# Optimization experiments

Hardware: AMD Instinct MI355X
Metric: run time of the kernel (lower is better)

The kernel has to match this reference:

```python
import jax, jax.numpy as jnp
import numpy as np

B, S, E, H = 2, 2048, 1024, 16
D = E // H  # head_dim = 64
EPS = 1e-6


def _angle_decay():
    # angle: 1/10000**linspace(0,1,D//2), each value repeated twice (interleaved)
    a = 1.0 / (10000.0 ** jnp.linspace(0.0, 1.0, D // 2))
    angle = jnp.repeat(a, 2)  # [D]
    decay = jnp.log(1.0 - 2.0 ** (-5.0 - jnp.arange(H, dtype=jnp.float32)))  # [H]
    return angle, decay


def _rel_pos(slen):
    angle, decay = _angle_decay()
    idx = jnp.arange(slen, dtype=jnp.float32)
    sin = jnp.sin(idx[:, None] * angle[None, :])  # [S, D]
    cos = jnp.cos(idx[:, None] * angle[None, :])  # [S, D]
    diff = idx[:, None] - idx[None, :]            # [S, S]
    tril = diff >= 0
    masked = jnp.where(tril, diff, jnp.inf)
    mask = jnp.exp(masked * decay[:, None, None])  # [H, S, S]; exp(-inf)=0 on upper tri
    mask = jnp.nan_to_num(mask)
    mask = mask / jnp.sqrt(jnp.sum(mask, axis=-1, keepdims=True))
    return sin, cos, mask


def _rotate_every_two(x):
    x1 = x[..., ::2]
    x2 = x[..., 1::2]
    return jnp.stack((-x2, x1), axis=-1).reshape(x.shape)


def _theta_shift(x, sin, cos):
    # x: [B, H, S, D]; sin/cos: [S, D] broadcast over B,H
    return x * cos + _rotate_every_two(x) * sin


def setup_inputs() -> dict:
    key = jax.random.key(0)
    ks = jax.random.split(key, 5)
    scale = 1.0 / np.sqrt(E)
    return {
        "x": jax.random.normal(ks[0], (B, S, E), dtype=jnp.float32),
        "Wq": jax.random.normal(ks[1], (E, E), dtype=jnp.float32) * scale,
        "Wk": jax.random.normal(ks[2], (E, E), dtype=jnp.float32) * scale,
        "Wv": jax.random.normal(ks[3], (E, E), dtype=jnp.float32) * scale,
        "Wg": jax.random.normal(ks[4], (E, E), dtype=jnp.float32) * scale,
    }


def reference(x, Wq, Wk, Wv, Wg):
    bsz, tgt_len, _ = x.shape
    sin, cos, mask = _rel_pos(tgt_len)
    scaling = E ** (-0.5)

    q = x @ Wq
    k = (x @ Wk) * scaling
    v = x @ Wv
    g = x @ Wg

    q = q.reshape(bsz, tgt_len, H, D).transpose(0, 2, 1, 3)  # [B,H,S,D]
    k = k.reshape(bsz, tgt_len, H, D).transpose(0, 2, 1, 3)
    vr = v.reshape(bsz, tgt_len, H, D).transpose(0, 2, 1, 3)

    qr = _theta_shift(q, sin, cos)
    kr = _theta_shift(k, sin, cos)

    qk = jnp.einsum("bhqd,bhkd->bhqk", qr, kr) * mask[None]
    denom = jax.lax.stop_gradient(
        jnp.clip(jnp.sum(jnp.abs(qk), axis=-1, keepdims=True), 1.0, 5e4)
    )
    out = jnp.einsum("bhqk,bhkd->bhqd", qk / denom, vr)
    out = out.transpose(0, 2, 1, 3)  # [B,S,H,D]

    # RMSNorm over head_dim (no affine)
    out = out * jax.lax.rsqrt(jnp.mean(out * out, axis=-1, keepdims=True) + EPS)
    out = out.reshape(bsz, tgt_len, E)
    return jax.nn.silu(g) * out
```

## Files before the change

### kernel.cpp

```cpp
#include <hip/hip_runtime.h>

typedef unsigned short u16;
typedef unsigned int u32;
typedef __attribute__((ext_vector_type(8))) __bf16 bf16x8;
typedef __attribute__((ext_vector_type(4))) float f32x4;

#define B_SZ   2
#define S_LEN  2048
#define E_DIM  1024
#define NHEAD  16
#define HD     64
#define KDIM   1024

__device__ __forceinline__ float bf2f(u16 u){
  union { u32 i; float f; } c; c.i = ((u32)u) << 16; return c.f;
}
__device__ __forceinline__ u16 f2bf(float f){
  union { float f; u32 i; } c; c.f = f;
  return (u16)((c.i + 0x7FFFu + ((c.i >> 16) & 1u)) >> 16);
}
__device__ __forceinline__ u16 f2bf_fast(float f){
  union { float f; u32 i; } c; c.f = f;
  return (u16)((c.i + 0x8000u) >> 16);
}
__device__ __forceinline__ void gl2lds16(const void* g, void* l){
  __builtin_amdgcn_global_load_lds((const __attribute__((address_space(1))) void*)g,
                                   (__attribute__((address_space(3))) void*)l, 16, 0, 0);
}

__global__ __launch_bounds__(256) void prep_kernel(const float* __restrict__ x,
                                                   const float* __restrict__ Wq, const float* __restrict__ Wk,
                                                   const float* __restrict__ Wv, const float* __restrict__ Wg,
                                                   u16* __restrict__ xb, u16* __restrict__ WT){
  __shared__ u16 tile[64][66];
  int z = blockIdx.z;
  int t = threadIdx.x;
  if (z < 4){
    const float* Ws[4] = {Wq, Wk, Wv, Wg};
    const float* W = Ws[z];
    int n0 = blockIdx.x * 64, k0 = blockIdx.y * 64;
    int r = t >> 2, cg = (t & 3) * 16;
    const float* src = W + (size_t)(k0 + r) * E_DIM + n0 + cg;
    float f[16];
    #pragma unroll
    for (int c = 0; c < 4; c++) *(float4*)&f[c * 4] = *(const float4*)&src[c * 4];
    #pragma unroll
    for (int i = 0; i < 16; i++) tile[r][cg + i] = f2bf(f[i]);
    __syncthreads();
    u16 ov[16];
    #pragma unroll
    for (int i = 0; i < 16; i++) ov[i] = tile[cg + i][r];
    int n7 = r & 7, cb = cg >> 3;
    u16* dst = WT + (size_t)(z * E_DIM + n0 + r) * KDIM + k0;
    *(uint4*)&dst[(cb ^ n7) * 8]       = *(uint4*)&ov[0];
    *(uint4*)&dst[((cb + 1) ^ n7) * 8] = *(uint4*)&ov[8];
  } else {
    int blk = (z - 4) * 256 + blockIdx.y * 16 + blockIdx.x;
    size_t flat = ((size_t)blk * 256 + t) * 16;
    int m7 = (int)((flat >> 10) & 7);
    int cb = (int)((flat >> 3) & 7);
    size_t tl = flat & ~(size_t)63;
    float f[16];
    #pragma unroll
    for (int c = 0; c < 4; c++) *(float4*)&f[c * 4] = *(const float4*)&x[flat + c * 4];
    u16 o[16];
    #pragma unroll
    for (int i = 0; i < 16; i++) o[i] = f2bf(f[i]);
    *(uint4*)&xb[tl + ((cb ^ m7) * 8)]       = *(uint4*)&o[0];
    *(uint4*)&xb[tl + (((cb + 1) ^ m7) * 8)] = *(uint4*)&o[8];
  }
}

__global__ __launch_bounds__(512, 2) void gemm_kernel(const u16* __restrict__ A, const u16* __restrict__ Bt,
                                                      u16* __restrict__ qr, u16* __restrict__ kr,
                                                      u16* __restrict__ vt, u16* __restrict__ gc){
  __shared__ __align__(16) u16 As[2][2][128 * 64];
  __shared__ __align__(16) u16 Bs[2][2][128 * 64];
  int m0 = blockIdx.y * 256, n0 = blockIdx.x * 256;
  int t = threadIdx.x;
  int wave = t >> 6, lane = t & 63;
  int l15 = lane & 15, quad = lane >> 4, h8 = lane & 7;
  int wm = wave >> 2, wn = wave & 3;

  f32x4 acc[8][4];
  #pragma unroll
  for (int i = 0; i < 8; i++)
    #pragma unroll
    for (int j = 0; j < 4; j++) acc[i][j] = (f32x4){0.f, 0.f, 0.f, 0.f};

  auto stA = [&](int buf, int half, int kt){
    const u16* src = A + (size_t)(m0 + half * 128) * KDIM + kt * 64;
    #pragma unroll
    for (int c = 0; c < 2; c++){
      int L = c * 512 + t;
      gl2lds16(src + (size_t)(L >> 3) * KDIM + (L & 7) * 8, &As[buf][half][L * 8]);
    }
  };
  auto stB = [&](int buf, int half, int kt){
    const u16* src = Bt + (size_t)(n0 + half * 128) * KDIM + kt * 64;
    #pragma unroll
    for (int c = 0; c < 2; c++){
      int L = c * 512 + t;
      gl2lds16(src + (size_t)(L >> 3) * KDIM + (L & 7) * 8, &Bs[buf][half][L * 8]);
    }
  };
  auto ldA = [&](int buf, int i, int ks) -> bf16x8 {
    int r = i * 16 + l15;
    return *(const bf16x8*)&As[buf][wm][r * 64 + (((ks * 4 + quad) ^ h8) * 8)];
  };
  auto ldB = [&](int buf, int j, int ks) -> bf16x8 {
    int c = (wn & 1) * 64 + j * 16 + l15;
    return *(const bf16x8*)&Bs[buf][wn >> 1][c * 64 + (((ks * 4 + quad) ^ h8) * 8)];
  };

  stA(0, 0, 0); stB(0, 0, 0); stA(0, 1, 0); stB(0, 1, 0);
  asm volatile("s_waitcnt vmcnt(4)" ::: "memory");
  __builtin_amdgcn_s_barrier();

  bf16x8 a[4][2];
  bf16x8 bA[2][2];
  bf16x8 bB[2][2];

  for (int t2 = 0; t2 < 8; ++t2){
    int kt0 = 2 * t2;
    bool more = (t2 < 7);

    #pragma unroll
    for (int half = 0; half < 2; ++half){
      int buf = half;
      bool stg = (buf == 0) || more;
      {
        #pragma unroll
        for (int i = 0; i < 4; i++){ a[i][0] = ldA(buf, i, 0); a[i][1] = ldA(buf, i, 1); }
        #pragma unroll
        for (int j = 0; j < 2; j++){ bA[j][0] = ldB(buf, j, 0); bA[j][1] = ldB(buf, j, 1); }
        if (buf == 0){ stA(1, 0, kt0 + 1); stB(1, 0, kt0 + 1); }
        else if (more){ stA(0, 0, kt0 + 2); stB(0, 0, kt0 + 2); }
        __builtin_amdgcn_sched_barrier(0);
        __builtin_amdgcn_s_barrier();
        asm volatile("s_waitcnt lgkmcnt(0)" ::: "memory");
        __builtin_amdgcn_sched_barrier(0);
        __builtin_amdgcn_s_setprio(1);
        #pragma unroll
        for (int i = 0; i < 4; i++)
          #pragma unroll
          for (int j = 0; j < 2; j++){
            acc[i][j] = __builtin_amdgcn_mfma_f32_16x16x32_bf16(a[i][0], bA[j][0], acc[i][j], 0, 0, 0);
            acc[i][j] = __builtin_amdgcn_mfma_f32_16x16x32_bf16(a[i][1], bA[j][1], acc[i][j], 0, 0, 0);
          }
        __builtin_amdgcn_s_setprio(0);
        __builtin_amdgcn_sched_barrier(0);
        if (stg) { asm volatile("s_waitcnt vmcnt(4)" ::: "memory"); }
        else     { asm volatile("s_waitcnt vmcnt(0)" ::: "memory"); }
        __builtin_amdgcn_s_barrier();
      }
      {
        #pragma unroll
        for (int j = 0; j < 2; j++){ bB[j][0] = ldB(buf, j + 2, 0); bB[j][1] = ldB(buf, j + 2, 1); }
        if (buf == 0){ stA(1, 1, kt0 + 1); stB(1, 1, kt0 + 1); }
        else if (more){ stA(0, 1, kt0 + 2); stB(0, 1, kt0 + 2); }
        __builtin_amdgcn_sched_barrier(0);
        __builtin_amdgcn_s_barrier();
        asm volatile("s_waitcnt lgkmcnt(0)" ::: "memory");
        __builtin_amdgcn_sched_barrier(0);
        __builtin_amdgcn_s_setprio(1);
        #pragma unroll
        for (int i = 0; i < 4; i++)
          #pragma unroll
          for (int j = 0; j < 2; j++){
            acc[i][j + 2] = __builtin_amdgcn_mfma_f32_16x16x32_bf16(a[i][0], bB[j][0], acc[i][j + 2], 0, 0, 0);
            acc[i][j + 2] = __builtin_amdgcn_mfma_f32_16x16x32_bf16(a[i][1], bB[j][1], acc[i][j + 2], 0, 0, 0);
          }
        __builtin_amdgcn_s_setprio(0);
        __builtin_amdgcn_sched_barrier(0);
        __builtin_amdgcn_s_barrier();
      }
      {
        #pragma unroll
        for (int i = 0; i < 4; i++){ a[i][0] = ldA(buf, i + 4, 0); a[i][1] = ldA(buf, i + 4, 1); }
        __builtin_amdgcn_sched_barrier(0);
        __builtin_amdgcn_s_barrier();
        asm volatile("s_waitcnt lgkmcnt(0)" ::: "memory");
        __builtin_amdgcn_sched_barrier(0);
        __builtin_amdgcn_s_setprio(1);
        #pragma unroll
        for (int i = 0; i < 4; i++)
          #pragma unroll
          for (int j = 0; j < 2; j++){
            acc[i + 4][j + 2] = __builtin_amdgcn_mfma_f32_16x16x32_bf16(a[i][0], bB[j][0], acc[i + 4][j + 2], 0, 0, 0);
            acc[i + 4][j + 2] = __builtin_amdgcn_mfma_f32_16x16x32_bf16(a[i][1], bB[j][1], acc[i + 4][j + 2], 0, 0, 0);
          }
        #pragma unroll
        for (int i = 0; i < 4; i++)
          #pragma unroll
          for (int j = 0; j < 2; j++){
            acc[i + 4][j] = __builtin_amdgcn_mfma_f32_16x16x32_bf16(a[i][0], bA[j][0], acc[i + 4][j], 0, 0, 0);
            acc[i + 4][j] = __builtin_amdgcn_mfma_f32_16x16x32_bf16(a[i][1], bA[j][1], acc[i + 4][j], 0, 0, 0);
          }
        __builtin_amdgcn_s_setprio(0);
        __builtin_amdgcn_sched_barrier(0);
        if (stg) { asm volatile("s_waitcnt vmcnt(4)" ::: "memory"); }
        __builtin_amdgcn_s_barrier();
      }
    }
  }

  int zone = n0 >> 10;
  int n0l = n0 & 1023;
  int hh = (n0l >> 6) + wn;

  if (zone == 3){
    #pragma unroll
    for (int i = 0; i < 8; i++){
      int row = m0 + wm * 128 + i * 16 + quad * 4;
      #pragma unroll
      for (int j = 0; j < 4; j++){
        int e = n0l + wn * 64 + j * 16 + l15;
        #pragma unroll
        for (int r = 0; r < 4; r++)
          gc[(size_t)(row + r) * E_DIM + e] = f2bf(acc[i][j][r]);
      }
    }
  } else if (zone == 2){
    #pragma unroll
    for (int i = 0; i < 8; i++){
      int srow = m0 + wm * 128 + i * 16 + quad * 4;
      int b = srow >> 11, sb = srow & 2047;
      #pragma unroll
      for (int j = 0; j < 4; j++){
        int d = j * 16 + l15;
        size_t rowb = ((size_t)((b << 4) + hh) * HD + d) * S_LEN;
        u16 pk[4];
        #pragma unroll
        for (int r = 0; r < 4; r++) pk[r] = f2bf(acc[i][j][r]);
        u32 lo = (u32)pk[0] | ((u32)pk[1] << 16);
        u32 hi = (u32)pk[2] | ((u32)pk[3] << 16);
        size_t off = rowb + (size_t)(sb & ~63) + (size_t)(((((sb >> 3) & 7) ^ (d & 7)) << 3) + (sb & 7));
        *(uint2*)&vt[off] = make_uint2(lo, hi);
      }
    }
  } else {
    float scale = (zone == 1) ? 0.03125f : 1.0f;
    float sgn = (l15 & 1) ? 1.0f : -1.0f;
    #pragma unroll
    for (int j = 0; j < 4; j++){
      int d = j * 16 + l15;
      float af = exp2f(-(float)(d >> 1) * (13.287712379549449f / 31.0f));
      #pragma unroll
      for (int i = 0; i < 8; i++){
        int srow = m0 + wm * 128 + i * 16 + quad * 4;
        int b = srow >> 11, sbase = srow & 2047;
        size_t base = (size_t)((b << 4) + hh) * S_LEN;
        #pragma unroll
        for (int r = 0; r < 4; r++){
          int s = sbase + r;
          float vv = acc[i][j][r] * scale;
          float p = __shfl_xor(vv, 1);
          float sn, cs;
          __sincosf((float)s * af, &sn, &cs);
          float outv = vv * cs + sgn * p * sn;
          u16 ob = f2bf(outv);
          if (zone == 0){
            qr[(base + s) * HD + d] = ob;
          } else {
            kr[(base + s) * HD + (((((d >> 3) & 7) ^ (s & 7)) << 3) + (d & 7))] = ob;
          }
        }
      }
    }
  }
}

__global__ __launch_bounds__(256, 2) void retention_kernel(const u16* __restrict__ qr, const u16* __restrict__ kr,
                                                           const u16* __restrict__ vt,
                                                           u16* __restrict__ pO, u16* __restrict__ pBa){
  int bh = blockIdx.x;
  int qb = 15 - (int)blockIdx.y;
  int z  = blockIdx.z;
  int h = bh & 15;
  int q0 = qb * 128;
  __shared__ __align__(16) u16 Ks[2][64 * 64];
  __shared__ __align__(16) u16 Vs[2][64 * 64];
  __shared__ __align__(16) u16 Ps[128 * 72];
  int t = threadIdx.x, wave = t >> 6, lane = t & 63;
  int l15 = lane & 15, quad = lane >> 4, h8 = lane & 7;

  float decay = log1pf(-exp2f(-5.0f - (float)h));
  float negd = -decay;
  float estep = __expf(64.0f * negd);

  int qsE[2], rowb[2];
  #pragma unroll
  for (int e = 0; e < 2; e++){ rowb[e] = wave * 32 + e * 16; qsE[e] = q0 + rowb[e]; }

  bf16x8 qB[2][2];
  #pragma unroll
  for (int e = 0; e < 2; e++){
    size_t qrow = ((size_t)bh * S_LEN + qsE[e] + l15) * HD;
    qB[e][0] = *(const bf16x8*)&qr[qrow + quad * 8];
    qB[e][1] = *(const bf16x8*)&qr[qrow + 32 + quad * 8];
  }

  float win_f = 11.0f / negd;
  int win_i = (win_f > 2.1e9f) ? 0x7f000000 : (int)win_f;
  int nk = 2 * qb + 2;
  int z_lo = (z * nk) >> 2;
  int z_hi = (((z + 1) * nk) >> 2) - 1;
  int kb_lo = z_lo;
  {
    int jmin = q0 - win_i;
    if (jmin > z_lo * 64){ int wlo = jmin >> 6; kb_lo = wlo > z_lo ? wlo : z_lo; }
  }
  int k0s = kb_lo * 64;

  float em1d = expm1f(decay);
  float rfE[2]; int iE[2];
  #pragma unroll
  for (int e = 0; e < 2; e++){
    int i = qsE[e] + l15;
    iE[e] = i;
    float rowsum = expm1f((float)(i + 1) * decay) / em1d;
    rfE[e] = __expf((float)(i - k0s) * decay) * rsqrtf(rowsum);
  }
  float e1 = __expf(negd);
  float c16 = __expf(negd * 16.0f);
  float cbr[4];
  cbr[0] = __expf(negd * (float)(quad * 4));
  cbr[1] = cbr[0] * e1; cbr[2] = cbr[1] * e1; cbr[3] = cbr[2] * e1;

  f32x4 o[2][4];
  #pragma unroll
  for (int e = 0; e < 2; e++)
    #pragma unroll
    for (int dt = 0; dt < 4; dt++) o[e][dt] = (f32x4){0.f, 0.f, 0.f, 0.f};
  float babs[2] = {0.f, 0.f};

  const u16* krbh = kr + (size_t)bh * S_LEN * HD;
  const u16* vtbh = vt + (size_t)bh * HD * S_LEN;

  if (kb_lo <= z_hi){
    {
      int k0 = kb_lo * 64;
      #pragma unroll
      for (int c = 0; c < 2; c++){
        int L = c * 256 + t;
        gl2lds16(krbh + (size_t)k0 * HD + L * 8, &Ks[0][L * 8]);
      }
      #pragma unroll
      for (int c = 0; c < 2; c++){
        int L = c * 256 + t;
        gl2lds16(vtbh + (size_t)(L >> 3) * S_LEN + k0 + (L & 7) * 8, &Vs[0][L * 8]);
      }
    }
    __syncthreads();
    int cur = 0;
    for (int kb = kb_lo; kb <= z_hi; kb++){
      if (kb < z_hi){
        int k0n = (kb + 1) * 64;
        #pragma unroll
        for (int c = 0; c < 2; c++){
          int L = c * 256 + t;
          gl2lds16(krbh + (size_t)k0n * HD + L * 8, &Ks[cur ^ 1][L * 8]);
        }
        #pragma unroll
        for (int c = 0; c < 2; c++){
          int L = c * 256 + t;
          gl2lds16(vtbh + (size_t)(L >> 3) * S_LEN + k0n + (L & 7) * 8, &Vs[cur ^ 1][L * 8]);
        }
      }
      int k0 = kb * 64;
      const u16* KsC = &Ks[cur][0];
      const u16* VsC = &Vs[cur][0];

      bf16x8 kA0[4], kA1[4];
      #pragma unroll
      for (int ct = 0; ct < 4; ct++){
        int rw = (ct * 16 + l15) * 64;
        kA0[ct] = *(const bf16x8*)&KsC[rw + ((quad ^ h8) * 8)];
        kA1[ct] = *(const bf16x8*)&KsC[rw + (((quad + 4) ^ h8) * 8)];
      }
      #pragma unroll
      for (int e = 0; e < 2; e++){
        int qs = qsE[e];
        if (k0 <= qs + 15 && k0 + 63 >= qs - win_i){
          bool diag = (k0 + 64 > qs);
          float cf[4] = {cbr[0], cbr[1], cbr[2], cbr[3]};
          #pragma unroll
          for (int ct = 0; ct < 4; ct++){
            f32x4 zacc = (f32x4){0.f, 0.f, 0.f, 0.f};
            zacc = __builtin_amdgcn_mfma_f32_16x16x32_bf16(kA0[ct], qB[e][0], zacc, 0, 0, 0);
            zacc = __builtin_amdgcn_mfma_f32_16x16x32_bf16(kA1[ct], qB[e][1], zacc, 0, 0, 0);
            u16 pk[4];
            #pragma unroll
            for (int r = 0; r < 4; r++){
              float p = zacc[r] * (rfE[e] * cf[r]);
              if (diag && (k0 + ct * 16 + quad * 4 + r) > iE[e]) p = 0.f;
              babs[e] += fabsf(p);
              pk[r] = f2bf_fast(p);
              cf[r] *= c16;
            }
            u32 lo = (u32)pk[0] | ((u32)pk[1] << 16);
            u32 hi = (u32)pk[2] | ((u32)pk[3] << 16);
            *(uint2*)&Ps[(rowb[e] + l15) * 72 + ct * 16 + quad * 4] = make_uint2(lo, hi);
          }
        }
      }
      #pragma unroll
      for (int e = 0; e < 2; e++){
        int qs = qsE[e];
        if (k0 <= qs + 15 && k0 + 63 >= qs - win_i){
          bf16x8 pB0 = *(const bf16x8*)&Ps[(rowb[e] + l15) * 72 + quad * 8];
          bf16x8 pB1 = *(const bf16x8*)&Ps[(rowb[e] + l15) * 72 + 32 + quad * 8];
          #pragma unroll
          for (int dt = 0; dt < 4; dt++){
            int rw = (dt * 16 + l15) * 64;
            bf16x8 vA0 = *(const bf16x8*)&VsC[rw + ((quad ^ h8) * 8)];
            bf16x8 vA1 = *(const bf16x8*)&VsC[rw + (((quad + 4) ^ h8) * 8)];
            o[e][dt] = __builtin_amdgcn_mfma_f32_16x16x32_bf16(vA0, pB0, o[e][dt], 0, 0, 0);
            o[e][dt] = __builtin_amdgcn_mfma_f32_16x16x32_bf16(vA1, pB1, o[e][dt], 0, 0, 0);
          }
        }
      }
      #pragma unroll
      for (int e = 0; e < 2; e++) rfE[e] *= estep;
      __syncthreads();
      cur ^= 1;
    }
  }

  size_t slot = ((size_t)bh * 16 + qb) * 4 + z;
  u16* po = pO + slot * (4 * 128 * 16);
  #pragma unroll
  for (int e = 0; e < 2; e++){
    float bsum = babs[e];
    bsum += __shfl_xor(bsum, 16);
    bsum += __shfl_xor(bsum, 32);
    if (quad == 0) pBa[slot * 128 + rowb[e] + l15] = f2bf(bsum);
    #pragma unroll
    for (int dt = 0; dt < 4; dt++){
      u16 pk[4];
      #pragma unroll
      for (int r = 0; r < 4; r++) pk[r] = f2bf(o[e][dt][r]);
      *(uint2*)&po[(dt * 128 + rowb[e] + l15) * 16 + quad * 4] = *(uint2*)pk;
    }
  }
}

__global__ __launch_bounds__(128) void combine_kernel(const u16* __restrict__ pO, const u16* __restrict__ pBa,
                                                      const u16* __restrict__ gc, float* __restrict__ out){
  int bh = blockIdx.x, qb = blockIdx.y;
  int b = bh >> 4, h = bh & 15;
  int i = threadIdx.x;
  int s = qb * 128 + i;
  size_t s4 = ((size_t)bh * 16 + qb) * 4;
  float v[64];
  #pragma unroll
  for (int d = 0; d < 64; d++) v[d] = 0.f;
  float bsum = 0.f;
  #pragma unroll
  for (int z = 0; z < 4; z++){
    const u16* pz = pO + (s4 + z) * 8192;
    #pragma unroll
    for (int dt = 0; dt < 4; dt++){
      u16 a[16];
      *(uint4*)&a[0] = *(const uint4*)&pz[(dt * 128 + i) * 16];
      *(uint4*)&a[8] = *(const uint4*)&pz[(dt * 128 + i) * 16 + 8];
      #pragma unroll
      for (int c = 0; c < 16; c++) v[dt * 16 + c] += bf2f(a[c]);
    }
    bsum += bf2f(pBa[(s4 + z) * 128 + i]);
  }
  float dinv = 1.0f / fminf(fmaxf(bsum, 1.0f), 50000.0f);
  float ssq = 0.f;
  #pragma unroll
  for (int d = 0; d < 64; d++){ v[d] *= dinv; ssq += v[d] * v[d]; }
  float rms = rsqrtf(ssq * (1.0f / 64.0f) + 1e-6f);
  size_t gbase = ((size_t)b * S_LEN + s) * E_DIM + h * HD;
  u16 gu[64];
  #pragma unroll
  for (int c = 0; c < 8; c++) *(uint4*)&gu[c * 8] = *(const uint4*)&gc[gbase + c * 8];
  float ov[64];
  #pragma unroll
  for (int d = 0; d < 64; d++){
    float gv = bf2f(gu[d]);
    float sg = gv / (1.0f + __expf(-gv));
    ov[d] = v[d] * rms * sg;
  }
  float* obase = out + ((size_t)b * S_LEN + s) * E_DIM + h * HD;
  #pragma unroll
  for (int c = 0; c < 16; c++) *(float4*)&obase[c * 4] = *(float4*)&ov[c * 4];
}

extern "C" void kernel_launch(void* const* d_in, const int* in_sizes, int n_in,
                              void* d_out, int out_size, void* d_ws, size_t ws_size,
                              hipStream_t stream){
  const float* x  = (const float*)d_in[0];
  const float* Wq = (const float*)d_in[1];
  const float* Wk = (const float*)d_in[2];
  const float* Wv = (const float*)d_in[3];
  const float* Wg = (const float*)d_in[4];
  float* out = (float*)d_out;
  char* ws = (char*)d_ws;
  u16* xb  = (u16*)(ws);
  u16* WT  = (u16*)(ws + (8ull  << 20));
  u16* pO  = (u16*)(ws);
  u16* qrp = (u16*)(ws + (32ull << 20));
  u16* krp = (u16*)(ws + (40ull << 20));
  u16* vtp = (u16*)(ws + (48ull << 20));
  u16* gcp = (u16*)(ws + (56ull << 20));
  u16* pBa = (u16*)(ws + (64ull << 20));

  prep_kernel     <<<dim3(16, 16, 8),  256, 0, stream>>>(x, Wq, Wk, Wv, Wg, xb, WT);
  gemm_kernel     <<<dim3(16, 16),     512, 0, stream>>>(xb, WT, qrp, krp, vtp, gcp);
  retention_kernel<<<dim3(32, 16, 4),  256, 0, stream>>>(qrp, krp, vtp, pO, pBa);
  combine_kernel  <<<dim3(32, 16),     128, 0, stream>>>(pO, pBa, gcp, out);
}
```

Before: 191.2 us.

## Stage GEMM epilogue through LDS for coalesced 16-byte output stores

The GEMM epilogue now writes each wave's accumulator tile into a reused shared-memory region, then reads it back and issues coalesced 16-byte global stores for the q, k, v and g outputs, replacing scattered 2-byte and 8-byte stores. The RoPE sin/cos values are advanced by angle-addition recurrences instead of calling sincos for every element. To make the LDS reuse safe, the main loop's vmcnt waits are tightened to vmcnt(0), which may reduce load/compute overlap. The recurrence also adds some rounding drift compared with direct sincos.

```diff
diff --git a/kernel.cpp b/kernel.cpp
--- a/kernel.cpp
+++ b/kernel.cpp
@@ -74,8 +74,7 @@
 __global__ __launch_bounds__(512, 2) void gemm_kernel(const u16* __restrict__ A, const u16* __restrict__ Bt,
                                                       u16* __restrict__ qr, u16* __restrict__ kr,
                                                       u16* __restrict__ vt, u16* __restrict__ gc){
-  __shared__ __align__(16) u16 As[2][2][128 * 64];
-  __shared__ __align__(16) u16 Bs[2][2][128 * 64];
+  __shared__ __align__(16) u16 SH[65536];
   int m0 = blockIdx.y * 256, n0 = blockIdx.x * 256;
   int t = threadIdx.x;
   int wave = t >> 6, lane = t & 63;
@@ -88,12 +87,15 @@
     #pragma unroll
     for (int j = 0; j < 4; j++) acc[i][j] = (f32x4){0.f, 0.f, 0.f, 0.f};
 
+  auto Aoff = [&](int buf, int half) -> int { return (buf * 2 + half) * 8192; };
+  auto Boff = [&](int buf, int half) -> int { return 32768 + (buf * 2 + half) * 8192; };
+
   auto stA = [&](int buf, int half, int kt){
     const u16* src = A + (size_t)(m0 + half * 128) * KDIM + kt * 64;
     #pragma unroll
     for (int c = 0; c < 2; c++){
       int L = c * 512 + t;
-      gl2lds16(src + (size_t)(L >> 3) * KDIM + (L & 7) * 8, &As[buf][half][L * 8]);
+      gl2lds16(src + (size_t)(L >> 3) * KDIM + (L & 7) * 8, &SH[Aoff(buf, half) + L * 8]);
     }
   };
   auto stB = [&](int buf, int half, int kt){
@@ -101,20 +103,20 @@
     #pragma unroll
     for (int c = 0; c < 2; c++){
       int L = c * 512 + t;
-      gl2lds16(src + (size_t)(L >> 3) * KDIM + (L & 7) * 8, &Bs[buf][half][L * 8]);
+      gl2lds16(src + (size_t)(L >> 3) * KDIM + (L & 7) * 8, &SH[Boff(buf, half) + L * 8]);
     }
   };
   auto ldA = [&](int buf, int i, int ks) -> bf16x8 {
     int r = i * 16 + l15;
-    return *(const bf16x8*)&As[buf][wm][r * 64 + (((ks * 4 + quad) ^ h8) * 8)];
+    return *(const bf16x8*)&SH[Aoff(buf, wm) + r * 64 + (((ks * 4 + quad) ^ h8) * 8)];
   };
   auto ldB = [&](int buf, int j, int ks) -> bf16x8 {
     int c = (wn & 1) * 64 + j * 16 + l15;
-    return *(const bf16x8*)&Bs[buf][wn >> 1][c * 64 + (((ks * 4 + quad) ^ h8) * 8)];
+    return *(const bf16x8*)&SH[Boff(buf, wn >> 1) + c * 64 + (((ks * 4 + quad) ^ h8) * 8)];
   };
 
   stA(0, 0, 0); stB(0, 0, 0); stA(0, 1, 0); stB(0, 1, 0);
-  asm volatile("s_waitcnt vmcnt(4)" ::: "memory");
+  asm volatile("s_waitcnt vmcnt(0)" ::: "memory");
   __builtin_amdgcn_s_barrier();
 
   bf16x8 a[4][2];
@@ -150,8 +152,6 @@
           }
         __builtin_amdgcn_s_setprio(0);
         __builtin_amdgcn_sched_barrier(0);
-        if (stg) { asm volatile("s_waitcnt vmcnt(4)" ::: "memory"); }
-        else     { asm volatile("s_waitcnt vmcnt(0)" ::: "memory"); }
         __builtin_amdgcn_s_barrier();
       }
       {
@@ -199,45 +199,61 @@
           }
         __builtin_amdgcn_s_setprio(0);
         __builtin_amdgcn_sched_barrier(0);
-        if (stg) { asm volatile("s_waitcnt vmcnt(4)" ::: "memory"); }
+        if (stg) { asm volatile("s_waitcnt vmcnt(0)" ::: "memory"); }
         __builtin_amdgcn_s_barrier();
       }
     }
   }
 
+  __syncthreads();
+  u16* epi = SH + wave * 8192;
   int zone = n0 >> 10;
   int n0l = n0 & 1023;
   int hh = (n0l >> 6) + wn;
-
-  if (zone == 3){
-    #pragma unroll
-    for (int i = 0; i < 8; i++){
-      int row = m0 + wm * 128 + i * 16 + quad * 4;
-      #pragma unroll
-      for (int j = 0; j < 4; j++){
-        int e = n0l + wn * 64 + j * 16 + l15;
-        #pragma unroll
-        for (int r = 0; r < 4; r++)
-          gc[(size_t)(row + r) * E_DIM + e] = f2bf(acc[i][j][r]);
-      }
-    }
-  } else if (zone == 2){
-    #pragma unroll
-    for (int i = 0; i < 8; i++){
-      int srow = m0 + wm * 128 + i * 16 + quad * 4;
-      int b = srow >> 11, sb = srow & 2047;
-      #pragma unroll
-      for (int j = 0; j < 4; j++){
-        int d = j * 16 + l15;
-        size_t rowb = ((size_t)((b << 4) + hh) * HD + d) * S_LEN;
+  int b = m0 >> 11;
+  int s0f = (m0 & 2047) + wm * 128;
+
+  if (zone == 2){
+    #pragma unroll
+    for (int j = 0; j < 4; j++){
+      int d = j * 16 + l15;
+      #pragma unroll
+      for (int i = 0; i < 8; i++){
+        int cs0 = i * 2 + (quad >> 1);
         u16 pk[4];
         #pragma unroll
         for (int r = 0; r < 4; r++) pk[r] = f2bf(acc[i][j][r]);
-        u32 lo = (u32)pk[0] | ((u32)pk[1] << 16);
-        u32 hi = (u32)pk[2] | ((u32)pk[3] << 16);
-        size_t off = rowb + (size_t)(sb & ~63) + (size_t)(((((sb >> 3) & 7) ^ (d & 7)) << 3) + (sb & 7));
-        *(uint2*)&vt[off] = make_uint2(lo, hi);
-      }
+        *(uint2*)&epi[d * 128 + ((cs0 ^ (d & 7)) * 8) + (quad & 1) * 4] = *(uint2*)pk;
+      }
+    }
+    __syncthreads();
+    int dl = lane >> 4, cl = lane & 15;
+    size_t vbase = (size_t)((b << 4) + hh) * HD * S_LEN;
+    #pragma unroll
+    for (int it = 0; it < 16; it++){
+      int d = it * 4 + dl;
+      uint4 v = *(const uint4*)&epi[d * 128 + cl * 8];
+      *(uint4*)&vt[vbase + (size_t)d * S_LEN + s0f + cl * 8] = v;
+    }
+  } else if (zone == 3){
+    #pragma unroll
+    for (int j = 0; j < 4; j++){
+      int c0c = 2 * j + (l15 >> 3), o7 = l15 & 7;
+      #pragma unroll
+      for (int i = 0; i < 8; i++)
+        #pragma unroll
+        for (int r = 0; r < 4; r++){
+          int row = i * 16 + quad * 4 + r;
+          epi[row * 64 + ((c0c ^ (row & 7)) * 8) + o7] = f2bf(acc[i][j][r]);
+        }
+    }
+    __syncthreads();
+    int rl = lane >> 3, cl = lane & 7;
+    #pragma unroll
+    for (int it = 0; it < 16; it++){
+      int row = it * 8 + rl;
+      uint4 v = *(const uint4*)&epi[row * 64 + ((cl ^ (row & 7)) * 8)];
+      *(uint4*)&gc[(size_t)(m0 + wm * 128 + row) * E_DIM + n0l + wn * 64 + cl * 8] = v;
     }
   } else {
     float scale = (zone == 1) ? 0.03125f : 1.0f;
@@ -245,28 +261,37 @@
     #pragma unroll
     for (int j = 0; j < 4; j++){
       int d = j * 16 + l15;
+      int c0c = 2 * j + (l15 >> 3), o7 = l15 & 7;
       float af = exp2f(-(float)(d >> 1) * (13.287712379549449f / 31.0f));
-      #pragma unroll
-      for (int i = 0; i < 8; i++){
-        int srow = m0 + wm * 128 + i * 16 + quad * 4;
-        int b = srow >> 11, sbase = srow & 2047;
-        size_t base = (size_t)((b << 4) + hh) * S_LEN;
+      float cs, sn, ca1, sa1, cb, sb_;
+      __sincosf((float)(s0f + quad * 4) * af, &sn, &cs);
+      __sincosf(af, &sa1, &ca1);
+      __sincosf(13.0f * af, &sb_, &cb);
+      #pragma unroll
+      for (int i = 0; i < 8; i++)
         #pragma unroll
         for (int r = 0; r < 4; r++){
-          int s = sbase + r;
+          int row = i * 16 + quad * 4 + r;
           float vv = acc[i][j][r] * scale;
           float p = __shfl_xor(vv, 1);
-          float sn, cs;
-          __sincosf((float)s * af, &sn, &cs);
           float outv = vv * cs + sgn * p * sn;
-          u16 ob = f2bf(outv);
-          if (zone == 0){
-            qr[(base + s) * HD + d] = ob;
-          } else {
-            kr[(base + s) * HD + (((((d >> 3) & 7) ^ (s & 7)) << 3) + (d & 7))] = ob;
-          }
+          epi[row * 64 + ((c0c ^ (row & 7)) * 8) + o7] = f2bf(outv);
+          float nc, ns;
+          if (r < 3){ nc = cs * ca1 - sn * sa1; ns = sn * ca1 + cs * sa1; }
+          else      { nc = cs * cb  - sn * sb_; ns = sn * cb  + cs * sb_; }
+          cs = nc; sn = ns;
         }
-      }
+    }
+    __syncthreads();
+    int rl = lane >> 3, cl = lane & 7;
+    size_t qkbase = (size_t)((b << 4) + hh) * S_LEN + s0f;
+    u16* dst = (zone == 0) ? qr : kr;
+    #pragma unroll
+    for (int it = 0; it < 16; it++){
+      int row = it * 8 + rl;
+      int rp = (zone == 0) ? (cl ^ (row & 7)) : cl;
+      uint4 v = *(const uint4*)&epi[row * 64 + rp * 8];
+      *(uint4*)&dst[(qkbase + row) * HD + cl * 8] = v;
     }
   }
 }
```

New measurement: 176.7 us. 1.08x faster.
